# Kernel optimization log

Measured on AMD Instinct MI355X. Metric: run time of the kernel, lower is better.

The kernel has to match this reference:

```python
import jax, jax.numpy as jnp
import numpy as np

B, L, D, F = 8, 1024, 256, 11
TEMP = D ** 0.5
LN_EPS = 1e-6


def setup_inputs() -> dict:
    key = jax.random.key(0)
    ks = jax.random.split(key, 14)
    mk = lambda k, s: jax.random.normal(k, s, dtype=jnp.float32)
    return {
        "q": mk(ks[0], (B, L, D)),
        "k": mk(ks[1], (B, L, D)),
        "v": mk(ks[2], (B, L, D)),
        "x": jax.random.uniform(ks[3], (B, L, F), dtype=jnp.float32),
        "inputs_lengths": jax.random.randint(ks[4], (B,), 512, L + 1),
        "w_qs": mk(ks[5], (D, D)) * 0.05,
        "w_ks": mk(ks[6], (D, D)) * 0.05,
        "w_vs": mk(ks[7], (D, D)) * 0.05,
        "w_qs2": mk(ks[8], (D, D)) * 0.05,
        "w_ks2": mk(ks[9], (D, D)) * 0.05,
        "w_fc": mk(ks[10], (D, D)) * 0.05,
        "feature_importance": mk(ks[11], (F,)) * 0.1,
        "ln_gamma": jnp.ones((D,), jnp.float32),
        "ln_beta": jnp.zeros((D,), jnp.float32),
    }


def reference(q, k, v, x, w_qs, w_ks, w_vs, w_qs2, w_ks2, w_fc,
              feature_importance, ln_gamma, ln_beta, inputs_lengths):
    lin = lambda a, w: jnp.einsum('bli,oi->blo', a, w)  # torch Linear: y = x W^T
    qp = lin(q, w_qs)
    kp = lin(k, w_ks)
    vp = lin(v, w_vs)
    q2 = lin(q, w_qs2)
    k2 = lin(k, w_ks2)

    # key-position validity mask [B, L]
    key_mask = jnp.arange(L)[None, :] < inputs_lengths[:, None]

    # FeatureSim: pairwise L1 feature distances weighted by feature_importance
    fd = jnp.abs(x[:, :, None, :] - x[:, None, :, :])           # [B,L,L,F]
    fa = jnp.einsum('bijf,f->bij', fd, feature_importance)      # [B,L,L]
    fa = jnp.where(key_mask[:, None, :], fa, -jnp.inf)          # pad_masking
    fa = jax.nn.softmax(fa, axis=-1)
    fa = jnp.nan_to_num(fa)                                     # nan -> 0 for fully-masked rows

    # dual-score attention with tanh activation (no row normalization)
    attn = jnp.einsum('bid,bjd->bij', qp / TEMP, kp)
    q2f = jnp.einsum('bij,bjd->bid', fa, q2)
    k2f = jnp.einsum('bij,bjd->bid', fa, k2)
    attn = attn + jnp.einsum('bid,bjd->bij', q2f / TEMP, k2f)
    zm = key_mask[:, None, :]
    attn = jnp.where(zm, attn, 0.0)                             # pad_zero_masking
    attn = jnp.tanh(attn)
    attn = jnp.where(zm, attn, 0.0)                             # pad_zero_masking (tanh(0)=0, kept for fidelity)

    out = jnp.einsum('bij,bjd->bid', attn, vp)
    out = lin(out, w_fc) + q                                    # dropout is identity at eval
    mu = jnp.mean(out, axis=-1, keepdims=True)
    var = jnp.var(out, axis=-1, keepdims=True)
    out = (out - mu) / jnp.sqrt(var + LN_EPS) * ln_gamma + ln_beta
    return (out, attn)
```

## Files before the change

### kernel.cpp

```cpp
#include <hip/hip_runtime.h>
#include <hip/hip_bf16.h>
#include <math.h>

typedef __hip_bfloat16 bf16;
typedef __bf16 bf16x8 __attribute__((ext_vector_type(8)));
typedef float  f32x4  __attribute__((ext_vector_type(4)));

#define NB 8
#define SL 1024
#define DD 256
#define NF 11
#define RPB 8

#define AS_G __attribute__((address_space(1)))
#define AS_L __attribute__((address_space(3)))

__device__ __forceinline__ bf16x8 ldfrag(const bf16* p) {
  return *reinterpret_cast<const bf16x8*>(p);
}
__device__ __forceinline__ bf16x8 ldfrag(const float* p) {
  const float4 a = *reinterpret_cast<const float4*>(p);
  const float4 b = *reinterpret_cast<const float4*>(p + 4);
  bf16x8 r;
  r[0] = (__bf16)a.x; r[1] = (__bf16)a.y; r[2] = (__bf16)a.z; r[3] = (__bf16)a.w;
  r[4] = (__bf16)b.x; r[5] = (__bf16)b.y; r[6] = (__bf16)b.z; r[7] = (__bf16)b.w;
  return r;
}
__device__ __forceinline__ unsigned short us(float f) {
  bf16 h = __float2bfloat16(f);
  return *reinterpret_cast<unsigned short*>(&h);
}
__device__ __forceinline__ float tanh_fast(float x) {
  return 1.f - 2.f / (__expf(2.f * x) + 1.f);
}

template<int R>
__device__ __forceinline__ void stage_t(const float* __restrict__ g, int ld,
                                        bf16* __restrict__ s, int tid) {
#pragma unroll
  for (int it = 0; it < R / 32; ++it) {
    const int cid = it * 256 + tid;
    const int row = cid >> 3, c16 = cid & 7;
    bf16x8 v = ldfrag(g + (size_t)row * ld + c16 * 8);
    *reinterpret_cast<bf16x8*>(s + row * 64 + ((c16 ^ (row & 7)) << 3)) = v;
  }
}
template<int R>
__device__ __forceinline__ void stage_t(const bf16* __restrict__ g, int ld,
                                        bf16* __restrict__ s, int tid) {
  const int wbase = tid & ~63;
#pragma unroll
  for (int it = 0; it < R / 32; ++it) {
    const int cid = it * 256 + tid;
    const int row = cid >> 3, sc = cid & 7;
    const int c16 = sc ^ (row & 7);
    const bf16* src = g + (size_t)row * ld + c16 * 8;
    bf16* dst = s + (size_t)(it * 256 + wbase) * 8;
    __builtin_amdgcn_global_load_lds((const AS_G void*)src, (AS_L void*)dst, 16, 0, 0);
  }
}

__device__ __forceinline__ void compute_128x128(const bf16* __restrict__ sA,
                                                const bf16* __restrict__ sB,
                                                int lane, int wave, f32x4 acc[4][4]) {
  const int n15 = lane & 15, quad = lane >> 4;
  const int wr = (wave >> 1) << 6, wc = (wave & 1) << 6;
#pragma unroll
  for (int kc = 0; kc < 2; ++kc) {
    const int c16 = kc * 4 + quad;
    bf16x8 aF[4], bF[4];
#pragma unroll
    for (int t = 0; t < 4; ++t) {
      const int ra = wr + t * 16 + n15;
      aF[t] = *reinterpret_cast<const bf16x8*>(sA + ra * 64 + ((c16 ^ (ra & 7)) << 3));
      const int rb = wc + t * 16 + n15;
      bF[t] = *reinterpret_cast<const bf16x8*>(sB + rb * 64 + ((c16 ^ (rb & 7)) << 3));
    }
#pragma unroll
    for (int ti = 0; ti < 4; ++ti)
#pragma unroll
      for (int tj = 0; tj < 4; ++tj)
        acc[ti][tj] = __builtin_amdgcn_mfma_f32_16x16x32_bf16(aF[ti], bF[tj], acc[ti][tj], 0, 0, 0);
  }
}

template<typename TA, typename TB>
__device__ __forceinline__ void gemm_128x128(const TA* __restrict__ A, int lda,
                                             const TB* __restrict__ B, int ldb, int K,
                                             bf16* s, int tid, f32x4 acc[4][4]) {
  const int lane = tid & 63, wave = tid >> 6;
  stage_t<128>(A, lda, s, tid);
  stage_t<128>(B, ldb, s + 8192, tid);
  int cur = 0;
  __syncthreads();
  for (int k0 = 0; k0 < K; k0 += 64) {
    bf16* sc0 = s + cur * 16384;
    if (k0 + 64 < K) {
      bf16* sn = s + (cur ^ 1) * 16384;
      stage_t<128>(A + k0 + 64, lda, sn, tid);
      stage_t<128>(B + k0 + 64, ldb, sn + 8192, tid);
    }
    compute_128x128(sc0, sc0 + 8192, lane, wave, acc);
    __syncthreads();
    cur ^= 1;
  }
}

__device__ __forceinline__ float wred_sum(float v) {
#pragma unroll
  for (int o = 32; o > 0; o >>= 1) v += __shfl_xor(v, o, 64);
  return v;
}

__global__ __launch_bounds__(256) void k_prep(const float* __restrict__ q,
                                              const float* __restrict__ k,
                                              const float* __restrict__ v,
                                              const float* __restrict__ wfc,
                                              const float* __restrict__ wvs,
                                              bf16* __restrict__ cq,
                                              bf16* __restrict__ ck,
                                              bf16* __restrict__ cv,
                                              float* __restrict__ Wc)
{
  const int bid = blockIdx.x, tid = threadIdx.x;
  if (bid < 1536) {
    const int which = bid >> 9, sub = bid & 511;
    const float* src = (which == 0) ? q : (which == 1) ? k : v;
    bf16* dst = (which == 0) ? cq : (which == 1) ? ck : cv;
    const size_t base = (size_t)sub * 4096;
#pragma unroll
    for (int it = 0; it < 4; ++it) {
      const size_t off = base + (size_t)(it * 256 + tid) * 4;
      const float4 a = *reinterpret_cast<const float4*>(src + off);
      ushort4 pk = make_ushort4(us(a.x), us(a.y), us(a.z), us(a.w));
      *reinterpret_cast<ushort4*>(dst + off) = pk;
    }
  } else {
    const int o = bid - 1536, m = tid;
    const float* fr = wfc + (size_t)o * DD;
    float acc = 0.f;
#pragma unroll 8
    for (int i = 0; i < DD; ++i)
      acc += fr[i] * wvs[(size_t)i * DD + m];
    Wc[(size_t)o * DD + m] = acc;
  }
}

__global__ __launch_bounds__(256) void k_proj(
    const bf16* __restrict__ cq, const bf16* __restrict__ ck, const bf16* __restrict__ cv,
    const float* __restrict__ wqs, const float* __restrict__ wks, const float* __restrict__ Wc,
    const float* __restrict__ wqs2, const float* __restrict__ wks2,
    bf16* __restrict__ qq, bf16* __restrict__ kk,
    bf16* __restrict__ vpwt, bf16* __restrict__ q2t, bf16* __restrict__ k2t)
{
  __shared__ bf16 smem[32768];
  const int tid = threadIdx.x, lane = tid & 63, wave = tid >> 6;
  const int z = blockIdx.z;
  const bf16*  A = (z == 2) ? cv : ((z == 1 || z == 4) ? ck : cq);
  const float* W = (z == 0) ? wqs : (z == 1) ? wks : (z == 2) ? Wc : (z == 3) ? wqs2 : wks2;
  const int rowBase = blockIdx.x * 128;
  const int colBase = blockIdx.y * 128;
  f32x4 acc[4][4] = {};
  gemm_128x128(A + (size_t)rowBase * DD, DD, W + (size_t)colBase * DD, DD, DD, smem, tid, acc);
  const int n15 = lane & 15, quad = lane >> 4;
  const int wr = (wave >> 1) << 6, wc = (wave & 1) << 6;
  if (z <= 1) {
    bf16* O = (z == 0) ? qq : kk;
#pragma unroll
    for (int ti = 0; ti < 4; ++ti)
#pragma unroll
      for (int tj = 0; tj < 4; ++tj)
#pragma unroll
        for (int r = 0; r < 4; ++r) {
          int row = rowBase + wr + ti * 16 + quad * 4 + r;
          int col = colBase + wc + tj * 16 + n15;
          O[(size_t)row * 512 + col] = __float2bfloat16(acc[ti][tj][r]);
        }
  } else {
    bf16* O = (z == 2) ? vpwt : (z == 3) ? q2t : k2t;
    const int bb = rowBase >> 10, rowInB = rowBase & 1023;
#pragma unroll
    for (int ti = 0; ti < 4; ++ti)
#pragma unroll
      for (int tj = 0; tj < 4; ++tj) {
        int l0  = rowInB + wr + ti * 16 + quad * 4;
        int col = colBase + wc + tj * 16 + n15;
        ushort4 pk = make_ushort4(us(acc[ti][tj][0]), us(acc[ti][tj][1]),
                                  us(acc[ti][tj][2]), us(acc[ti][tj][3]));
        *reinterpret_cast<ushort4*>(&O[((size_t)bb * DD + col) * SL + l0]) = pk;
      }
  }
}

__global__ __launch_bounds__(256) void k_fa(const float* __restrict__ x,
                                            const float* __restrict__ fi_g,
                                            const int* __restrict__ lens,
                                            bf16* __restrict__ fa)
{
  __shared__ __align__(16) float sx[SL * NF];
  __shared__ float sredS[4][RPB];
  const int tid = threadIdx.x, wave = tid >> 6;
  const int b  = blockIdx.x >> 7;
  const int i0 = (blockIdx.x & 127) * RPB;
  {
    const float4* src = reinterpret_cast<const float4*>(x + (size_t)b * SL * NF);
    float4* dst = reinterpret_cast<float4*>(sx);
#pragma unroll
    for (int it = 0; it < 11; ++it) dst[it * 256 + tid] = src[it * 256 + tid];
  }
  float fiv[NF];
#pragma unroll
  for (int f = 0; f < NF; ++f) fiv[f] = fi_g[f];
  const int len = lens[b];
  __syncthreads();
  float xi[RPB][NF];
#pragma unroll
  for (int i = 0; i < RPB; ++i)
#pragma unroll
    for (int f = 0; f < NF; ++f) xi[i][f] = sx[(i0 + i) * NF + f];
  float e[RPB][4];
  float ps[RPB];
#pragma unroll
  for (int i = 0; i < RPB; ++i) ps[i] = 0.f;
#pragma unroll
  for (int t = 0; t < 4; ++t) {
    const int j = tid + t * 256;
    const bool valid = (t < 2) || (j < len);
    float xj[NF];
#pragma unroll
    for (int f = 0; f < NF; ++f) xj[f] = sx[j * NF + f];
#pragma unroll
    for (int i = 0; i < RPB; ++i) {
      float a = 0.f;
#pragma unroll
      for (int f = 0; f < NF; ++f) a += fabsf(xi[i][f] - xj[f]) * fiv[f];
      float ev = valid ? __expf(a) : 0.f;
      e[i][t] = ev;
      ps[i] += ev;
    }
  }
#pragma unroll
  for (int i = 0; i < RPB; ++i) {
    float wsv = wred_sum(ps[i]);
    if ((tid & 63) == 0) sredS[wave][i] = wsv;
  }
  __syncthreads();
  bf16* out = fa + (size_t)b * SL * SL + (size_t)i0 * SL;
#pragma unroll
  for (int i = 0; i < RPB; ++i) {
    const float inv = 1.f / (sredS[0][i] + sredS[1][i] + sredS[2][i] + sredS[3][i]);
#pragma unroll
    for (int t = 0; t < 4; ++t)
      out[(size_t)i * SL + tid + t * 256] = __float2bfloat16(e[i][t] * inv);
  }
}

__global__ __launch_bounds__(256) void k_famul(const bf16* __restrict__ fa,
                                               const bf16* __restrict__ q2t,
                                               const bf16* __restrict__ k2t,
                                               const int* __restrict__ lens,
                                               bf16* __restrict__ qq,
                                               bf16* __restrict__ kk)
{
  __shared__ bf16 smem[32768];
  const int tid = threadIdx.x, lane = tid & 63, wave = tid >> 6;
  const int flat = blockIdx.x + 8 * blockIdx.y + 16 * blockIdx.z;
  const int lid  = (flat & 7) * 32 + (flat >> 3);
  const int bx = lid & 7, by = (lid >> 3) & 1, bz = lid >> 4;
  const int b = bz >> 1, which = bz & 1;
  const int iBase = bx * 128, dBase = by * 128;
  const int Keff = (lens[b] + 63) & ~63;
  const bf16* A  = fa + (size_t)b * SL * SL + (size_t)iBase * SL;
  const bf16* Bm = (which ? k2t : q2t) + (size_t)b * DD * SL + (size_t)dBase * SL;
  f32x4 acc[4][4] = {};
  gemm_128x128(A, SL, Bm, SL, Keff, smem, tid, acc);
  bf16* O = (which ? kk : qq) + (size_t)b * SL * 512 + 256;
  const int n15 = lane & 15, quad = lane >> 4;
  const int wr = (wave >> 1) << 6, wc = (wave & 1) << 6;
#pragma unroll
  for (int ti = 0; ti < 4; ++ti)
#pragma unroll
    for (int tj = 0; tj < 4; ++tj)
#pragma unroll
      for (int r = 0; r < 4; ++r)
        O[(size_t)(iBase + wr + ti * 16 + quad * 4 + r) * 512 +
          dBase + wc + tj * 16 + n15] = __float2bfloat16(acc[ti][tj][r]);
}

__global__ __launch_bounds__(256) void k_attn(const bf16* __restrict__ qq,
                                              const bf16* __restrict__ kk,
                                              const int* __restrict__ lens,
                                              float* __restrict__ attn_f32,
                                              bf16* __restrict__ attn_b16)
{
  __shared__ bf16 smem[32768];
  const int tid = threadIdx.x, lane = tid & 63, wave = tid >> 6;
  const int flat = blockIdx.x + 8 * blockIdx.y + 64 * blockIdx.z;
  const int lid  = (flat & 7) * 64 + (flat >> 3);
  const int bx = lid & 7, by = (lid >> 3) & 7, bz = lid >> 6;
  const int b = bz;
  const int iBase = bx * 128, jBase = by * 128;
  const int len = lens[b];
  if (jBase >= len) {
    const int r = tid >> 1, ch = (tid & 1) * 64;
    float* pf = attn_f32 + (size_t)b * SL * SL + (size_t)(iBase + r) * SL + jBase + ch;
    bf16*  pb = attn_b16 + (size_t)b * SL * SL + (size_t)(iBase + r) * SL + jBase + ch;
    const float4 z4 = make_float4(0.f, 0.f, 0.f, 0.f);
    const uint4  zb = make_uint4(0u, 0u, 0u, 0u);
#pragma unroll
    for (int i = 0; i < 16; ++i) *reinterpret_cast<float4*>(pf + i * 4) = z4;
#pragma unroll
    for (int i = 0; i < 8; ++i)  *reinterpret_cast<uint4*>(pb + i * 8) = zb;
    return;
  }
  f32x4 acc[4][4] = {};
  gemm_128x128(qq + ((size_t)b * SL + iBase) * 512, 512,
               kk + ((size_t)b * SL + jBase) * 512, 512, 512, smem, tid, acc);
  const int n15 = lane & 15, quad = lane >> 4;
  const int wr = (wave >> 1) << 6, wc = (wave & 1) << 6;
#pragma unroll
  for (int ti = 0; ti < 4; ++ti)
#pragma unroll
    for (int tj = 0; tj < 4; ++tj)
#pragma unroll
      for (int r = 0; r < 4; ++r) {
        int i = iBase + wr + ti * 16 + quad * 4 + r;
        int j = jBase + wc + tj * 16 + n15;
        float vv = (j < len) ? tanh_fast(acc[ti][tj][r] * (1.f / 16.f)) : 0.f;
        size_t idx = (size_t)b * SL * SL + (size_t)i * SL + j;
        attn_f32[idx] = vv;
        attn_b16[idx] = __float2bfloat16(vv);
      }
}

__global__ __launch_bounds__(256) void k_av(const bf16* __restrict__ attn,
                                            const bf16* __restrict__ vpwt,
                                            const float* __restrict__ qres,
                                            const int* __restrict__ lens,
                                            float* __restrict__ fcout)
{
  __shared__ bf16 smem[32768];
  const int tid = threadIdx.x, lane = tid & 63, wave = tid >> 6;
  const int flat = blockIdx.x + 8 * blockIdx.y + 16 * blockIdx.z;
  const int lid  = (flat & 7) * 16 + (flat >> 3);
  const int bx = lid & 7, by = (lid >> 3) & 1, bz = lid >> 4;
  const int b = bz;
  const int iBase = bx * 128, dBase = by * 128;
  const int Keff = (lens[b] + 63) & ~63;
  f32x4 acc[4][4] = {};
  gemm_128x128(attn + (size_t)b * SL * SL + (size_t)iBase * SL, SL,
               vpwt + (size_t)b * DD * SL + (size_t)dBase * SL, SL, Keff, smem, tid, acc);
  const int n15 = lane & 15, quad = lane >> 4;
  const int wr = (wave >> 1) << 6, wc = (wave & 1) << 6;
#pragma unroll
  for (int ti = 0; ti < 4; ++ti)
#pragma unroll
    for (int tj = 0; tj < 4; ++tj)
#pragma unroll
      for (int r = 0; r < 4; ++r) {
        size_t row = (size_t)b * SL + iBase + wr + ti * 16 + quad * 4 + r;
        int col = dBase + wc + tj * 16 + n15;
        fcout[row * DD + col] = acc[ti][tj][r] + qres[row * DD + col];
      }
}

__global__ __launch_bounds__(256) void k_ln(const float* __restrict__ fcout,
                                            const float* __restrict__ gam,
                                            const float* __restrict__ bet,
                                            float* __restrict__ outp)
{
  __shared__ float r1[4], r2[4];
  const int r = blockIdx.x, tid = threadIdx.x;
  const float v = fcout[(size_t)r * DD + tid];
  float s = wred_sum(v), ss = wred_sum(v * v);
  if ((tid & 63) == 0) { r1[tid >> 6] = s; r2[tid >> 6] = ss; }
  __syncthreads();
  s  = r1[0] + r1[1] + r1[2] + r1[3];
  ss = r2[0] + r2[1] + r2[2] + r2[3];
  const float mean = s * (1.f / DD);
  const float var  = ss * (1.f / DD) - mean * mean;
  float y = (v - mean) * rsqrtf(var + 1e-6f);
  y = y * gam[tid] + bet[tid];
  outp[(size_t)r * DD + tid] = y;
}

extern "C" void kernel_launch(void* const* d_in, const int* in_sizes, int n_in,
                              void* d_out, int out_size, void* d_ws, size_t ws_size,
                              hipStream_t stream)
{
  const float* q    = (const float*)d_in[0];
  const float* k    = (const float*)d_in[1];
  const float* v    = (const float*)d_in[2];
  const float* x    = (const float*)d_in[3];
  const int*  lens  = (const int*)d_in[4];
  const float* wqs  = (const float*)d_in[5];
  const float* wks  = (const float*)d_in[6];
  const float* wvs  = (const float*)d_in[7];
  const float* wqs2 = (const float*)d_in[8];
  const float* wks2 = (const float*)d_in[9];
  const float* wfc  = (const float*)d_in[10];
  const float* fi   = (const float*)d_in[11];
  const float* gam  = (const float*)d_in[12];
  const float* bet  = (const float*)d_in[13];

  char* w = (char*)d_ws;
  const size_t MB = 1u << 20;
  const size_t KB = 1u << 10;
  bf16* qq    = (bf16*)(w + 0 * MB);
  bf16* kk    = (bf16*)(w + 8 * MB);
  bf16* vpwt  = (bf16*)(w + 16 * MB);
  bf16* q2t   = (bf16*)(w + 20 * MB);
  bf16* k2t   = (bf16*)(w + 24 * MB);
  bf16* cq    = (bf16*)(w + 28 * MB);
  bf16* ck    = (bf16*)(w + 32 * MB);
  bf16* cv    = (bf16*)(w + 36 * MB);
  float* Wc   = (float*)(w + 40 * MB);
  bf16* fa    = (bf16*)(w + 28 * MB);
  bf16* attn_b16 = fa;
  float* fcout = (float*)(w + 0 * MB);

  float* outp  = (float*)d_out;
  float* attnp = outp + (size_t)NB * SL * DD;
  (void)KB; (void)wvs;

  dim3 blk(256);
  hipLaunchKernelGGL(k_prep,  dim3(1792),      blk, 0, stream, q, k, v, wfc, wvs,
                     cq, ck, cv, Wc);
  hipLaunchKernelGGL(k_proj,  dim3(64, 2, 5),  blk, 0, stream,
                     cq, ck, cv, wqs, wks, Wc, wqs2, wks2, qq, kk, vpwt, q2t, k2t);
  hipLaunchKernelGGL(k_fa,    dim3(NB * 128),  blk, 0, stream, x, fi, lens, fa);
  hipLaunchKernelGGL(k_famul, dim3(8, 2, 16),  blk, 0, stream, fa, q2t, k2t, lens, qq, kk);
  hipLaunchKernelGGL(k_attn,  dim3(8, 8, 8),   blk, 0, stream,
                     qq, kk, lens, attnp, attn_b16);
  hipLaunchKernelGGL(k_av,    dim3(8, 2, 8),   blk, 0, stream, attn_b16, vpwt, q, lens, fcout);
  hipLaunchKernelGGL(k_ln,    dim3(NB * SL),   blk, 0, stream, fcout, gam, bet, outp);
}
```

Before: 200.6 us.

## Fuse LayerNorm into AV GEMM, merge FA with Wc prep, drop bf16 casts

The separate q/k/v bf16 conversion pass is removed, and the projection GEMM now reads fp32 inputs directly through the float ldfrag path. The feature-similarity softmax kernel is merged with the Wc = Wfc·Wvs precompute, which now computes four output rows per block. The AV GEMM is retiled to 32x256 so each block owns full rows, letting it add the residual and apply LayerNorm in its epilogue instead of writing fcout and launching a separate LN kernel. This removes two launches and an fp32 intermediate round trip. In exchange, the AV stage runs only 256 blocks, and each block restages the whole V tile, which cuts parallelism and raises redundant loads.

```diff
diff --git a/kernel.cpp b/kernel.cpp
--- a/kernel.cpp
+++ b/kernel.cpp
@@ -78,6 +78,33 @@
     }
 #pragma unroll
     for (int ti = 0; ti < 4; ++ti)
+#pragma unroll
+      for (int tj = 0; tj < 4; ++tj)
+        acc[ti][tj] = __builtin_amdgcn_mfma_f32_16x16x32_bf16(aF[ti], bF[tj], acc[ti][tj], 0, 0, 0);
+  }
+}
+
+__device__ __forceinline__ void compute_32x256(const bf16* __restrict__ sA,
+                                               const bf16* __restrict__ sB,
+                                               int lane, int wave, f32x4 acc[2][4]) {
+  const int n15 = lane & 15, quad = lane >> 4;
+  const int wc = wave << 6;
+#pragma unroll
+  for (int kc = 0; kc < 2; ++kc) {
+    const int c16 = kc * 4 + quad;
+    bf16x8 aF[2], bF[4];
+#pragma unroll
+    for (int t = 0; t < 2; ++t) {
+      const int ra = t * 16 + n15;
+      aF[t] = *reinterpret_cast<const bf16x8*>(sA + ra * 64 + ((c16 ^ (ra & 7)) << 3));
+    }
+#pragma unroll
+    for (int t = 0; t < 4; ++t) {
+      const int rb = wc + t * 16 + n15;
+      bF[t] = *reinterpret_cast<const bf16x8*>(sB + rb * 64 + ((c16 ^ (rb & 7)) << 3));
+    }
+#pragma unroll
+    for (int ti = 0; ti < 2; ++ti)
 #pragma unroll
       for (int tj = 0; tj < 4; ++tj)
         acc[ti][tj] = __builtin_amdgcn_mfma_f32_16x16x32_bf16(aF[ti], bF[tj], acc[ti][tj], 0, 0, 0);
@@ -112,42 +139,93 @@
   return v;
 }
 
-__global__ __launch_bounds__(256) void k_prep(const float* __restrict__ q,
-                                              const float* __restrict__ k,
-                                              const float* __restrict__ v,
+__global__ __launch_bounds__(256) void k_fawc(const float* __restrict__ x,
+                                              const float* __restrict__ fi_g,
+                                              const int* __restrict__ lens,
                                               const float* __restrict__ wfc,
                                               const float* __restrict__ wvs,
-                                              bf16* __restrict__ cq,
-                                              bf16* __restrict__ ck,
-                                              bf16* __restrict__ cv,
+                                              bf16* __restrict__ fa,
                                               float* __restrict__ Wc)
 {
-  const int bid = blockIdx.x, tid = threadIdx.x;
-  if (bid < 1536) {
-    const int which = bid >> 9, sub = bid & 511;
-    const float* src = (which == 0) ? q : (which == 1) ? k : v;
-    bf16* dst = (which == 0) ? cq : (which == 1) ? ck : cv;
-    const size_t base = (size_t)sub * 4096;
-#pragma unroll
-    for (int it = 0; it < 4; ++it) {
-      const size_t off = base + (size_t)(it * 256 + tid) * 4;
-      const float4 a = *reinterpret_cast<const float4*>(src + off);
-      ushort4 pk = make_ushort4(us(a.x), us(a.y), us(a.z), us(a.w));
-      *reinterpret_cast<ushort4*>(dst + off) = pk;
-    }
-  } else {
-    const int o = bid - 1536, m = tid;
-    const float* fr = wfc + (size_t)o * DD;
-    float acc = 0.f;
+  __shared__ __align__(16) float sx[SL * NF];
+  __shared__ float sredS[4][RPB];
+  const int tid = threadIdx.x, wave = tid >> 6;
+  const int bid = blockIdx.x;
+  if (bid >= NB * 128) {
+    const int o0 = (bid - NB * 128) * 4, m = tid;
+    const float* f0 = wfc + (size_t)o0 * DD;
+    float a0 = 0.f, a1 = 0.f, a2 = 0.f, a3 = 0.f;
 #pragma unroll 8
-    for (int i = 0; i < DD; ++i)
-      acc += fr[i] * wvs[(size_t)i * DD + m];
-    Wc[(size_t)o * DD + m] = acc;
+    for (int i = 0; i < DD; ++i) {
+      const float wv = wvs[(size_t)i * DD + m];
+      a0 += f0[i] * wv;
+      a1 += f0[DD + i] * wv;
+      a2 += f0[2 * DD + i] * wv;
+      a3 += f0[3 * DD + i] * wv;
+    }
+    Wc[(size_t)(o0 + 0) * DD + m] = a0;
+    Wc[(size_t)(o0 + 1) * DD + m] = a1;
+    Wc[(size_t)(o0 + 2) * DD + m] = a2;
+    Wc[(size_t)(o0 + 3) * DD + m] = a3;
+    return;
+  }
+  const int b  = bid >> 7;
+  const int i0 = (bid & 127) * RPB;
+  {
+    const float4* src = reinterpret_cast<const float4*>(x + (size_t)b * SL * NF);
+    float4* dst = reinterpret_cast<float4*>(sx);
+#pragma unroll
+    for (int it = 0; it < 11; ++it) dst[it * 256 + tid] = src[it * 256 + tid];
+  }
+  float fiv[NF];
+#pragma unroll
+  for (int f = 0; f < NF; ++f) fiv[f] = fi_g[f];
+  const int len = lens[b];
+  __syncthreads();
+  float xi[RPB][NF];
+#pragma unroll
+  for (int i = 0; i < RPB; ++i)
+#pragma unroll
+    for (int f = 0; f < NF; ++f) xi[i][f] = sx[(i0 + i) * NF + f];
+  float e[RPB][4];
+  float ps[RPB];
+#pragma unroll
+  for (int i = 0; i < RPB; ++i) ps[i] = 0.f;
+#pragma unroll
+  for (int t = 0; t < 4; ++t) {
+    const int j = tid + t * 256;
+    const bool valid = (t < 2) || (j < len);
+    float xj[NF];
+#pragma unroll
+    for (int f = 0; f < NF; ++f) xj[f] = sx[j * NF + f];
+#pragma unroll
+    for (int i = 0; i < RPB; ++i) {
+      float a = 0.f;
+#pragma unroll
+      for (int f = 0; f < NF; ++f) a += fabsf(xi[i][f] - xj[f]) * fiv[f];
+      float ev = valid ? __expf(a) : 0.f;
+      e[i][t] = ev;
+      ps[i] += ev;
+    }
+  }
+#pragma unroll
+  for (int i = 0; i < RPB; ++i) {
+    float wsv = wred_sum(ps[i]);
+    if ((tid & 63) == 0) sredS[wave][i] = wsv;
+  }
+  __syncthreads();
+  bf16* out = fa + (size_t)b * SL * SL + (size_t)i0 * SL;
+#pragma unroll
+  for (int i = 0; i < RPB; ++i) {
+    const float inv = 1.f / (sredS[0][i] + sredS[1][i] + sredS[2][i] + sredS[3][i]);
+#pragma unroll
+    for (int t = 0; t < 4; ++t)
+      out[(size_t)i * SL + tid + t * 256] = __float2bfloat16(e[i][t] * inv);
   }
 }
 
 __global__ __launch_bounds__(256) void k_proj(
-    const bf16* __restrict__ cq, const bf16* __restrict__ ck, const bf16* __restrict__ cv,
+    const float* __restrict__ q, const float* __restrict__ k, const float* __restrict__ v,
     const float* __restrict__ wqs, const float* __restrict__ wks, const float* __restrict__ Wc,
     const float* __restrict__ wqs2, const float* __restrict__ wks2,
     bf16* __restrict__ qq, bf16* __restrict__ kk,
@@ -156,7 +234,7 @@
   __shared__ bf16 smem[32768];
   const int tid = threadIdx.x, lane = tid & 63, wave = tid >> 6;
   const int z = blockIdx.z;
-  const bf16*  A = (z == 2) ? cv : ((z == 1 || z == 4) ? ck : cq);
+  const float* A = (z == 2) ? v : ((z == 1 || z == 4) ? k : q);
   const float* W = (z == 0) ? wqs : (z == 1) ? wks : (z == 2) ? Wc : (z == 3) ? wqs2 : wks2;
   const int rowBase = blockIdx.x * 128;
   const int colBase = blockIdx.y * 128;
@@ -189,69 +267,6 @@
                                   us(acc[ti][tj][2]), us(acc[ti][tj][3]));
         *reinterpret_cast<ushort4*>(&O[((size_t)bb * DD + col) * SL + l0]) = pk;
       }
-  }
-}
-
-__global__ __launch_bounds__(256) void k_fa(const float* __restrict__ x,
-                                            const float* __restrict__ fi_g,
-                                            const int* __restrict__ lens,
-                                            bf16* __restrict__ fa)
-{
-  __shared__ __align__(16) float sx[SL * NF];
-  __shared__ float sredS[4][RPB];
-  const int tid = threadIdx.x, wave = tid >> 6;
-  const int b  = blockIdx.x >> 7;
-  const int i0 = (blockIdx.x & 127) * RPB;
-  {
-    const float4* src = reinterpret_cast<const float4*>(x + (size_t)b * SL * NF);
-    float4* dst = reinterpret_cast<float4*>(sx);
-#pragma unroll
-    for (int it = 0; it < 11; ++it) dst[it * 256 + tid] = src[it * 256 + tid];
-  }
-  float fiv[NF];
-#pragma unroll
-  for (int f = 0; f < NF; ++f) fiv[f] = fi_g[f];
-  const int len = lens[b];
-  __syncthreads();
-  float xi[RPB][NF];
-#pragma unroll
-  for (int i = 0; i < RPB; ++i)
-#pragma unroll
-    for (int f = 0; f < NF; ++f) xi[i][f] = sx[(i0 + i) * NF + f];
-  float e[RPB][4];
-  float ps[RPB];
-#pragma unroll
-  for (int i = 0; i < RPB; ++i) ps[i] = 0.f;
-#pragma unroll
-  for (int t = 0; t < 4; ++t) {
-    const int j = tid + t * 256;
-    const bool valid = (t < 2) || (j < len);
-    float xj[NF];
-#pragma unroll
-    for (int f = 0; f < NF; ++f) xj[f] = sx[j * NF + f];
-#pragma unroll
-    for (int i = 0; i < RPB; ++i) {
-      float a = 0.f;
-#pragma unroll
-      for (int f = 0; f < NF; ++f) a += fabsf(xi[i][f] - xj[f]) * fiv[f];
-      float ev = valid ? __expf(a) : 0.f;
-      e[i][t] = ev;
-      ps[i] += ev;
-    }
-  }
-#pragma unroll
-  for (int i = 0; i < RPB; ++i) {
-    float wsv = wred_sum(ps[i]);
-    if ((tid & 63) == 0) sredS[wave][i] = wsv;
-  }
-  __syncthreads();
-  bf16* out = fa + (size_t)b * SL * SL + (size_t)i0 * SL;
-#pragma unroll
-  for (int i = 0; i < RPB; ++i) {
-    const float inv = 1.f / (sredS[0][i] + sredS[1][i] + sredS[2][i] + sredS[3][i]);
-#pragma unroll
-    for (int t = 0; t < 4; ++t)
-      out[(size_t)i * SL + tid + t * 256] = __float2bfloat16(e[i][t] * inv);
   }
 }
 
@@ -333,55 +348,100 @@
       }
 }
 
-__global__ __launch_bounds__(256) void k_av(const bf16* __restrict__ attn,
-                                            const bf16* __restrict__ vpwt,
-                                            const float* __restrict__ qres,
-                                            const int* __restrict__ lens,
-                                            float* __restrict__ fcout)
-{
-  __shared__ bf16 smem[32768];
+__global__ __launch_bounds__(256) void k_avln(const bf16* __restrict__ attn,
+                                              const bf16* __restrict__ vpwt,
+                                              const float* __restrict__ qres,
+                                              const int* __restrict__ lens,
+                                              const float* __restrict__ gam,
+                                              const float* __restrict__ bet,
+                                              float* __restrict__ outp)
+{
+  __shared__ bf16 smem[36864];
   const int tid = threadIdx.x, lane = tid & 63, wave = tid >> 6;
-  const int flat = blockIdx.x + 8 * blockIdx.y + 16 * blockIdx.z;
-  const int lid  = (flat & 7) * 16 + (flat >> 3);
-  const int bx = lid & 7, by = (lid >> 3) & 1, bz = lid >> 4;
-  const int b = bz;
-  const int iBase = bx * 128, dBase = by * 128;
+  const int flat = blockIdx.x;
+  const int lid  = (flat & 7) * 32 + (flat >> 3);
+  const int b = lid >> 5, bx = lid & 31;
+  const int iBase = bx * 32;
   const int Keff = (lens[b] + 63) & ~63;
-  f32x4 acc[4][4] = {};
-  gemm_128x128(attn + (size_t)b * SL * SL + (size_t)iBase * SL, SL,
-               vpwt + (size_t)b * DD * SL + (size_t)dBase * SL, SL, Keff, smem, tid, acc);
-  const int n15 = lane & 15, quad = lane >> 4;
-  const int wr = (wave >> 1) << 6, wc = (wave & 1) << 6;
-#pragma unroll
-  for (int ti = 0; ti < 4; ++ti)
-#pragma unroll
-    for (int tj = 0; tj < 4; ++tj)
+  const bf16* A  = attn + (size_t)b * SL * SL + (size_t)iBase * SL;
+  const bf16* Bm = vpwt + (size_t)b * DD * SL;
+  f32x4 acc[2][4] = {};
+  {
+    stage_t<32>(A, SL, smem, tid);
+    stage_t<256>(Bm, SL, smem + 2048, tid);
+    int cur = 0;
+    __syncthreads();
+    for (int k0 = 0; k0 < Keff; k0 += 64) {
+      bf16* sc = smem + cur * 18432;
+      if (k0 + 64 < Keff) {
+        bf16* sn = smem + (cur ^ 1) * 18432;
+        stage_t<32>(A + k0 + 64, SL, sn, tid);
+        stage_t<256>(Bm + k0 + 64, SL, sn + 2048, tid);
+      }
+      compute_32x256(sc, sc + 2048, lane, wave, acc);
+      __syncthreads();
+      cur ^= 1;
+    }
+  }
+  const int n15 = lane & 15, quad = lane >> 4;
+  const int wc = wave << 6;
+  float val[2][4][4];
+  float sS_p[2][4], sQ_p[2][4];
+#pragma unroll
+  for (int ti = 0; ti < 2; ++ti)
+#pragma unroll
+    for (int r = 0; r < 4; ++r) {
+      const size_t grow = (size_t)b * SL + iBase + ti * 16 + quad * 4 + r;
+      float s = 0.f, ss = 0.f;
+#pragma unroll
+      for (int tj = 0; tj < 4; ++tj) {
+        const int col = wc + tj * 16 + n15;
+        float vv = acc[ti][tj][r] + qres[grow * DD + col];
+        val[ti][tj][r] = vv;
+        s += vv; ss += vv * vv;
+      }
+      sS_p[ti][r] = s; sQ_p[ti][r] = ss;
+    }
+#pragma unroll
+  for (int o = 8; o > 0; o >>= 1)
+#pragma unroll
+    for (int ti = 0; ti < 2; ++ti)
 #pragma unroll
       for (int r = 0; r < 4; ++r) {
-        size_t row = (size_t)b * SL + iBase + wr + ti * 16 + quad * 4 + r;
-        int col = dBase + wc + tj * 16 + n15;
-        fcout[row * DD + col] = acc[ti][tj][r] + qres[row * DD + col];
-      }
-}
-
-__global__ __launch_bounds__(256) void k_ln(const float* __restrict__ fcout,
-                                            const float* __restrict__ gam,
-                                            const float* __restrict__ bet,
-                                            float* __restrict__ outp)
-{
-  __shared__ float r1[4], r2[4];
-  const int r = blockIdx.x, tid = threadIdx.x;
-  const float v = fcout[(size_t)r * DD + tid];
-  float s = wred_sum(v), ss = wred_sum(v * v);
-  if ((tid & 63) == 0) { r1[tid >> 6] = s; r2[tid >> 6] = ss; }
+        sS_p[ti][r] += __shfl_xor(sS_p[ti][r], o, 64);
+        sQ_p[ti][r] += __shfl_xor(sQ_p[ti][r], o, 64);
+      }
+  float* sS = (float*)smem;
+  float* sQ = sS + 4 * 32;
+  if (n15 == 0) {
+#pragma unroll
+    for (int ti = 0; ti < 2; ++ti)
+#pragma unroll
+      for (int r = 0; r < 4; ++r) {
+        const int rloc = ti * 16 + quad * 4 + r;
+        sS[wave * 32 + rloc] = sS_p[ti][r];
+        sQ[wave * 32 + rloc] = sQ_p[ti][r];
+      }
+  }
   __syncthreads();
-  s  = r1[0] + r1[1] + r1[2] + r1[3];
-  ss = r2[0] + r2[1] + r2[2] + r2[3];
-  const float mean = s * (1.f / DD);
-  const float var  = ss * (1.f / DD) - mean * mean;
-  float y = (v - mean) * rsqrtf(var + 1e-6f);
-  y = y * gam[tid] + bet[tid];
-  outp[(size_t)r * DD + tid] = y;
+#pragma unroll
+  for (int ti = 0; ti < 2; ++ti)
+#pragma unroll
+    for (int r = 0; r < 4; ++r) {
+      const int rloc = ti * 16 + quad * 4 + r;
+      const float s  = sS[rloc] + sS[32 + rloc] + sS[64 + rloc] + sS[96 + rloc];
+      const float ss = sQ[rloc] + sQ[32 + rloc] + sQ[64 + rloc] + sQ[96 + rloc];
+      const float mean = s * (1.f / DD);
+      const float var  = ss * (1.f / DD) - mean * mean;
+      const float rstd = rsqrtf(var + 1e-6f);
+      const size_t grow = (size_t)b * SL + iBase + rloc;
+#pragma unroll
+      for (int tj = 0; tj < 4; ++tj) {
+        const int col = wc + tj * 16 + n15;
+        const float y = (val[ti][tj][r] - mean) * rstd * gam[col] + bet[col];
+        outp[grow * DD + col] = y;
+      }
+    }
 }
 
 extern "C" void kernel_launch(void* const* d_in, const int* in_sizes, int n_in,
@@ -405,33 +465,27 @@
 
   char* w = (char*)d_ws;
   const size_t MB = 1u << 20;
-  const size_t KB = 1u << 10;
   bf16* qq    = (bf16*)(w + 0 * MB);
   bf16* kk    = (bf16*)(w + 8 * MB);
   bf16* vpwt  = (bf16*)(w + 16 * MB);
   bf16* q2t   = (bf16*)(w + 20 * MB);
   bf16* k2t   = (bf16*)(w + 24 * MB);
-  bf16* cq    = (bf16*)(w + 28 * MB);
-  bf16* ck    = (bf16*)(w + 32 * MB);
-  bf16* cv    = (bf16*)(w + 36 * MB);
-  float* Wc   = (float*)(w + 40 * MB);
   bf16* fa    = (bf16*)(w + 28 * MB);
   bf16* attn_b16 = fa;
-  float* fcout = (float*)(w + 0 * MB);
+  float* Wc   = (float*)(w + 44 * MB);
 
   float* outp  = (float*)d_out;
   float* attnp = outp + (size_t)NB * SL * DD;
-  (void)KB; (void)wvs;
+  (void)wvs;
 
   dim3 blk(256);
-  hipLaunchKernelGGL(k_prep,  dim3(1792),      blk, 0, stream, q, k, v, wfc, wvs,
-                     cq, ck, cv, Wc);
+  hipLaunchKernelGGL(k_fawc, dim3(NB * 128 + 64), blk, 0, stream,
+                     x, fi, lens, wfc, wvs, fa, Wc);
   hipLaunchKernelGGL(k_proj,  dim3(64, 2, 5),  blk, 0, stream,
-                     cq, ck, cv, wqs, wks, Wc, wqs2, wks2, qq, kk, vpwt, q2t, k2t);
-  hipLaunchKernelGGL(k_fa,    dim3(NB * 128),  blk, 0, stream, x, fi, lens, fa);
+                     q, k, v, wqs, wks, Wc, wqs2, wks2, qq, kk, vpwt, q2t, k2t);
   hipLaunchKernelGGL(k_famul, dim3(8, 2, 16),  blk, 0, stream, fa, q2t, k2t, lens, qq, kk);
   hipLaunchKernelGGL(k_attn,  dim3(8, 8, 8),   blk, 0, stream,
                      qq, kk, lens, attnp, attn_b16);
-  hipLaunchKernelGGL(k_av,    dim3(8, 2, 8),   blk, 0, stream, attn_b16, vpwt, q, lens, fcout);
-  hipLaunchKernelGGL(k_ln,    dim3(NB * SL),   blk, 0, stream, fcout, gam, bet, outp);
-}
+  hipLaunchKernelGGL(k_avln,  dim3(256),       blk, 0, stream,
+                     attn_b16, vpwt, q, lens, gam, bet, outp);
+}
```

New measurement: 187.0 us. -6.8%, faster.
